# Performance work log

Hardware: AMD Instinct MI355X
Metric: run time of the kernel (lower is better)

The kernel has to match this reference:

```python
import jax, jax.numpy as jnp
import numpy as np
from itertools import product

IM_SIZE = (256, 256)
GRID_SIZE = (512, 512)
NUMPOINTS = (6, 6)
TABLE_OVERSAMP = (1024, 1024)
N_SHIFT = (128.0, 128.0)
ALPHA = tuple(2.34 * j for j in NUMPOINTS)
NBATCH, NCOIL, KLEN = 2, 16, 262144


def _kaiser_bessel(u, J, alpha):
    # order-0 Kaiser-Bessel kernel, support |u| < J/2
    z = np.sqrt(np.maximum(1.0 - (2.0 * u / J) ** 2, 0.0))
    f = np.i0(alpha * z) / np.i0(alpha)
    return np.where(np.abs(u) < J / 2.0, f, 0.0)


def _build_table(J, L, alpha):
    # table of length J*L+1 sampling the kernel at offsets u=(idx-center)/L
    idx = np.arange(J * L + 1, dtype=np.float64)
    center = np.floor(J * L / 2)
    u = (idx - center) / L
    real = _kaiser_bessel(u, J, alpha)
    return np.stack([real, np.zeros_like(real)]).astype(np.float32)  # [2, J*L+1] (real/imag)


def setup_inputs() -> dict:
    key = jax.random.key(0)
    k1, k2 = jax.random.split(key)
    x = jax.random.normal(k1, (NBATCH, NCOIL, 2) + GRID_SIZE, dtype=jnp.float32)
    om = (jax.random.uniform(k2, (NBATCH, 2, KLEN), dtype=jnp.float32) - 0.5) * (2.0 * np.pi)
    table_0 = jnp.asarray(_build_table(NUMPOINTS[0], TABLE_OVERSAMP[0], ALPHA[0]))
    table_1 = jnp.asarray(_build_table(NUMPOINTS[1], TABLE_OVERSAMP[1], ALPHA[1]))
    return {"x": x, "om": om, "table_0": table_0, "table_1": table_1}


def _interp(x, om, table_0, table_1):
    # x: [B, C, 2, Kx, Ky] gridded k-space; om: [B, 2, M] radians/voxel
    B, C = x.shape[0], x.shape[1]
    Kx, Ky = GRID_SIZE
    J0, J1 = NUMPOINTS
    M = om.shape[2]
    L = jnp.array(TABLE_OVERSAMP, dtype=x.dtype)
    centers = (J0 * TABLE_OVERSAMP[0] // 2, J1 * TABLE_OVERSAMP[1] // 2)
    gsz = jnp.array(GRID_SIZE, dtype=x.dtype)

    xflat = x.reshape(B, C, 2, Kx * Ky)
    tm = om * gsz[None, :, None] / (2.0 * jnp.pi)  # [B,2,M] grid units
    # offset to first interpolation coefficient location (Fessler convention)
    koff = 1.0 + jnp.floor(tm - jnp.array(NUMPOINTS, x.dtype)[None, :, None] / 2.0)

    # all J0*J1 tensor-product offsets
    joffs = jnp.asarray(list(product(range(J0), range(J1))), dtype=x.dtype)  # [36, 2]

    def step(carry, joff):
        acc_r, acc_i = carry
        gridind = koff + joff[None, :, None]  # [B,2,M], exact integers as floats
        distind = jnp.round((tm - gridind) * L[None, :, None]).astype(jnp.int32)  # [B,2,M]
        c0r = table_0[0, distind[:, 0] + centers[0]]  # [B,M]
        c0i = table_0[1, distind[:, 0] + centers[0]]
        c1r = table_1[0, distind[:, 1] + centers[1]]
        c1i = table_1[1, distind[:, 1] + centers[1]]
        coef_r = c0r * c1r - c0i * c1i
        coef_i = c0r * c1i + c0i * c1r
        gi = gridind.astype(jnp.int32)
        arr_ind = jnp.mod(gi[:, 0], Kx) * Ky + jnp.mod(gi[:, 1], Ky)  # [B,M] flat grid index
        dat_r = jnp.take_along_axis(xflat[:, :, 0, :], arr_ind[:, None, :], axis=2)  # [B,C,M]
        dat_i = jnp.take_along_axis(xflat[:, :, 1, :], arr_ind[:, None, :], axis=2)
        acc_r = acc_r + coef_r[:, None, :] * dat_r - coef_i[:, None, :] * dat_i
        acc_i = acc_i + coef_r[:, None, :] * dat_i + coef_i[:, None, :] * dat_r
        return (acc_r, acc_i), None

    init = (jnp.zeros((B, C, M), x.dtype), jnp.zeros((B, C, M), x.dtype))
    (kr, ki), _ = jax.lax.scan(step, init, joffs)

    # fftshift phase: y = exp(1j * om . n_shift) * kdat
    ph = jnp.einsum('bdm,d->bm', om, jnp.array(N_SHIFT, dtype=x.dtype))
    pr, pi = jnp.cos(ph), jnp.sin(ph)
    yr = kr * pr[:, None, :] - ki * pi[:, None, :]
    yi = kr * pi[:, None, :] + ki * pr[:, None, :]
    return jnp.stack([yr, yi], axis=2)  # [B,C,2,M]


def reference(x, om, table_0, table_1):
    return _interp(x, om, table_0, table_1)
```

## Files before the change

kernel.cpp:

```cpp
#include <hip/hip_runtime.h>
#include <hip/hip_fp16.h>


#define KLEN      262144
#define GX        512
#define GY        512
#define NCOILS    16
#define NBATCH    2
#define TBL_LEN   6145
#define TBL_CTR   3072
#define PLANE     (GX*GY)
#define NPTS      (NBATCH*KLEN)
#define NBINS     2048
#define NBLK      256
#define PPB       2048
#define TBLKS     (NBATCH*PLANE/256)

#define TROWS     21
#define TQ        5

typedef _Float16 half2_t __attribute__((ext_vector_type(2)));
struct alignas(16) H8 { half2_t h[4]; };

#define WS_XT       0
#define WS_OSORT    33554432
#define WS_BHIST    33554432
#define WS_BTOT     67108864
#define WS_BBASE    (67108864+8192)
#define WS_INV      69206016
#define WS_SOM      71303168
#define WS_TOTAL    75497472

__device__ inline int point_bin(float om0, float om1)
{
    const float TWO_PI = 6.2831853071795864769f;
    const float tm0 = (om0 * 512.0f) / TWO_PI;
    const float tm1 = (om1 * 512.0f) / TWO_PI;
    const int cx = ((int)floorf(tm0)) & 511;
    const int cy = ((int)floorf(tm1)) & 511;
    return ((cx >> 4) << 5) | (cy >> 4);
}

template<int O>
__device__ inline half2_t qbc(half2_t v)
{
    int i;
    __builtin_memcpy(&i, &v, 4);
    i = __builtin_amdgcn_mov_dpp(i, (O | (O << 2) | (O << 4) | (O << 6)),
                                 0xf, 0xf, true);
    half2_t r;
    __builtin_memcpy(&r, &i, 4);
    return r;
}

__global__ __launch_bounds__(256) void transpose_hist(
    const float* __restrict__ x, float4* __restrict__ xt,
    const float* __restrict__ om, unsigned* __restrict__ blockHist)
{
    __shared__ float s[32][260];
    const int t = threadIdx.x;

    if (blockHist != nullptr && blockIdx.x >= TBLKS) {
        unsigned* h = (unsigned*)s;
        const int blk = blockIdx.x - TBLKS;
#pragma unroll
        for (int i = 0; i < NBINS / 256; ++i) h[t + i * 256] = 0u;
        __syncthreads();
#pragma unroll
        for (int i = 0; i < PPB / 256; ++i) {
            const int id = blk * PPB + i * 256 + t;
            const int b = id >> 18, m = id & (KLEN - 1);
            const float om0 = om[(size_t)(b * 2 + 0) * KLEN + m];
            const float om1 = om[(size_t)(b * 2 + 1) * KLEN + m];
            const int g = (b << 10) | point_bin(om0, om1);
            atomicAdd(&h[g], 1u);
        }
        __syncthreads();
#pragma unroll
        for (int i = 0; i < NBINS / 256; ++i) {
            const int bin = t + i * 256;
            blockHist[(size_t)bin * NBLK + blk] = h[bin];
        }
        return;
    }

    const int blk   = blockIdx.x;
    const int base  = blk * 256;
    const int b     = base >> 18;
    const int cell0 = base & (PLANE - 1);

    const float* xb = x + (size_t)b * 32 * PLANE + cell0;
#pragma unroll
    for (int i = 0; i < 8; ++i) {
        const int fidx = i * 256 + t;
        const int pl = fidx >> 6;
        const int j  = fidx & 63;
        const float4 v = *(const float4*)(xb + (size_t)pl * PLANE + j * 4);
        *(float4*)&s[pl][j * 4] = v;
    }
    __syncthreads();
#pragma unroll
    for (int i = 0; i < 4; ++i) {
        const int chunk = i * 256 + t;
        const int cell = chunk >> 2, q = chunk & 3;
        H8 rec;
#pragma unroll
        for (int cc = 0; cc < 4; ++cc) {
            const int c = q * 4 + cc;
            rec.h[cc] = half2_t{(_Float16)s[2 * c][cell],
                                (_Float16)s[2 * c + 1][cell]};
        }
        xt[((size_t)b * PLANE + cell0 + cell) * 4 + q] = *(const float4*)&rec;
    }
}

__global__ __launch_bounds__(256) void scan_bins(
    unsigned* __restrict__ blockHist, unsigned* __restrict__ binTotal)
{
    __shared__ unsigned partial[256];
    const int bin = blockIdx.x;
    const int t = threadIdx.x;
    const unsigned v = blockHist[(size_t)bin * NBLK + t];
    partial[t] = v;
    __syncthreads();
    for (int d = 1; d < 256; d <<= 1) {
        unsigned x = (t >= d) ? partial[t - d] : 0u;
        __syncthreads();
        partial[t] += x;
        __syncthreads();
    }
    blockHist[(size_t)bin * NBLK + t] = partial[t] - v;
    if (t == 255) binTotal[bin] = partial[255];
}

__global__ __launch_bounds__(1024) void scatter2(
    const float*    __restrict__ om,
    const unsigned* __restrict__ blockHist,
    const unsigned* __restrict__ btot,
    unsigned* __restrict__ bbase,
    unsigned* __restrict__ inv,
    float2* __restrict__ som)
{
    __shared__ unsigned h[NBINS];
    __shared__ unsigned bbs[NBINS];
    __shared__ unsigned part[1024];
    const int t = threadIdx.x, blk = blockIdx.x;

    unsigned v[2];
    unsigned s = 0;
#pragma unroll
    for (int i = 0; i < 2; ++i) { v[i] = btot[t * 2 + i]; s += v[i]; }
    part[t] = s;
#pragma unroll
    for (int i = 0; i < NBINS / 1024; ++i) h[t + i * 1024] = 0u;
    __syncthreads();
    for (int d = 1; d < 1024; d <<= 1) {
        unsigned x = (t >= d) ? part[t - d] : 0u;
        __syncthreads();
        part[t] += x;
        __syncthreads();
    }
    unsigned base = (t > 0) ? part[t - 1] : 0u;
    bbs[t * 2]     = base;
    bbs[t * 2 + 1] = base + v[0];
    if (blk == 0) {
        bbase[t * 2]     = base;
        bbase[t * 2 + 1] = base + v[0];
    }
    __syncthreads();

#pragma unroll
    for (int i = 0; i < PPB / 1024; ++i) {
        const int id = blk * PPB + i * 1024 + t;
        const int b = id >> 18, m = id & (KLEN - 1);
        const float om0 = om[(size_t)(b * 2 + 0) * KLEN + m];
        const float om1 = om[(size_t)(b * 2 + 1) * KLEN + m];
        const int g = (b << 10) | point_bin(om0, om1);
        const unsigned r = atomicAdd(&h[g], 1u);
        const unsigned pos = bbs[g] + blockHist[(size_t)g * NBLK + blk] + r;
        inv[id]  = pos;
        som[pos] = make_float2(om0, om1);
    }
}

__global__ __launch_bounds__(256) void interp_bins(
    const float2*   __restrict__ som,
    const float*    __restrict__ t0,
    const float*    __restrict__ t1,
    const float4*   __restrict__ xt,
    const unsigned* __restrict__ bbase,
    float4*         __restrict__ osort)
{
    __shared__ float4 tile[TROWS * TROWS * TQ];
    const int bin = blockIdx.x;
    const int t   = threadIdx.x;
    const int b   = bin >> 10;
    const int cx0 = ((bin >> 5) & 31) << 4;
    const int cy0 = (bin & 31) << 4;

    const unsigned p0  = bbase[bin];
    const unsigned p1e = (bin == NBINS - 1) ? (unsigned)NPTS : bbase[bin + 1];
    const int cnt = (int)(p1e - p0);

    const float4* rec = xt + ((size_t)b << 20);
    for (int f = t; f < TROWS * TROWS * 4; f += 256) {
        const int r = f >> 2, q = f & 3;
        const int row = r / TROWS;
        const int col = r - row * TROWS;
        const int gr = (cx0 - 2 + row) & 511;
        const int gc = (cy0 - 2 + col) & 511;
        tile[r * TQ + q] = rec[(((size_t)((gr << 9) | gc)) << 2) + q];
    }
    __syncthreads();

    const int lane = t & 3;
    for (int base = 0; base < cnt; base += 64) {
        const int idx = base + (t >> 2);
        if (idx >= cnt) continue;
        const int pos = (int)p0 + idx;

        const float2 o = som[pos];
        const float om0 = o.x, om1 = o.y;

        const float TWO_PI = 6.2831853071795864769f;
        const float tm0 = (om0 * 512.0f) / TWO_PI;
        const float tm1 = (om1 * 512.0f) / TWO_PI;

        const float koff0 = 1.0f + floorf(tm0 - 3.0f);
        const float koff1 = 1.0f + floorf(tm1 - 3.0f);
        const int   k0    = (int)koff0;
        const int   k1    = (int)koff1;

        float c0r[6], c0i[6];
        int   loff[6];
#pragma unroll
        for (int j = 0; j < 6; ++j) {
            const float g0 = koff0 + (float)j;
            const int   d0 = (int)rintf((tm0 - g0) * 1024.0f) + TBL_CTR;
            c0r[j] = t0[d0];
            c0i[j] = t0[TBL_LEN + d0];
            loff[j] = ((k1 + j - cy0 + 2) & 511) * TQ;
        }
        const int j1a = lane;
        const int j1b = (lane < 2) ? lane + 4 : lane;
        const int d1a = (int)rintf((tm1 - (koff1 + (float)j1a)) * 1024.0f) + TBL_CTR;
        const int d1b = (int)rintf((tm1 - (koff1 + (float)j1b)) * 1024.0f) + TBL_CTR;
        const float c1ra = t1[d1a], c1ia = t1[TBL_LEN + d1a];
        const float c1rb = t1[d1b], c1ib = t1[TBL_LEN + d1b];

        float acr[4] = {0.f, 0.f, 0.f, 0.f};
        float aci[4] = {0.f, 0.f, 0.f, 0.f};

#define KB_DO_J1(JJ, OWNER, PP1, PP2)                                         \
        do {                                                                  \
            const half2_t p1 = qbc<OWNER>(PP1);                               \
            const half2_t p2 = qbc<OWNER>(PP2);                               \
            const float4 raw = rowp[loff[JJ]];                                \
            const H8 v = *(const H8*)&raw;                                    \
            _Pragma("unroll")                                                 \
            for (int cc = 0; cc < 4; ++cc) {                                  \
                acr[cc] = __builtin_amdgcn_fdot2(v.h[cc], p1, acr[cc], false);\
                aci[cc] = __builtin_amdgcn_fdot2(v.h[cc], p2, aci[cc], false);\
            }                                                                 \
        } while (0)

#pragma unroll
        for (int j0 = 0; j0 < 6; ++j0) {
            const int rIdx = (k0 + j0 - cx0 + 2) & 511;
            const float4* rowp = &tile[rIdx * (TROWS * TQ) + lane];
            const float ar = c0r[j0], ai = c0i[j0];
            const float crA = ar * c1ra - ai * c1ia;
            const float ciA = ar * c1ia + ai * c1ra;
            const float crB = ar * c1rb - ai * c1ib;
            const float ciB = ar * c1ib + ai * c1rb;
            const half2_t pA1 = {(_Float16)crA, (_Float16)(-ciA)};
            const half2_t pA2 = {(_Float16)ciA, (_Float16)crA};
            const half2_t pB1 = {(_Float16)crB, (_Float16)(-ciB)};
            const half2_t pB2 = {(_Float16)ciB, (_Float16)crB};

            KB_DO_J1(0, 0, pA1, pA2);
            KB_DO_J1(1, 1, pA1, pA2);
            KB_DO_J1(2, 2, pA1, pA2);
            KB_DO_J1(3, 3, pA1, pA2);
            KB_DO_J1(4, 0, pB1, pB2);
            KB_DO_J1(5, 1, pB1, pB2);
        }
#undef KB_DO_J1

        const float ph = om0 * 128.0f + om1 * 128.0f;
        const float s = __sinf(ph), c = __cosf(ph);

        H8 outrec;
#pragma unroll
        for (int cc = 0; cc < 4; ++cc) {
            const float yr = acr[cc] * c - aci[cc] * s;
            const float yi = acr[cc] * s + aci[cc] * c;
            outrec.h[cc] = half2_t{(_Float16)yr, (_Float16)yi};
        }
        osort[(size_t)pos * 4 + lane] = *(const float4*)&outrec;
    }
}

__global__ __launch_bounds__(256) void unsort_kernel(
    const unsigned* __restrict__ inv,
    const float4*   __restrict__ osort,
    float*          __restrict__ out)
{
    const int id = blockIdx.x * blockDim.x + threadIdx.x;
    const int b = id >> 18, m = id & (KLEN - 1);
    const unsigned pos = inv[id];
    const float4* rp = osort + (size_t)pos * 4;

    float4 raw[4];
#pragma unroll
    for (int q = 0; q < 4; ++q) raw[q] = rp[q];

    float* ob = out + (size_t)b * NCOILS * 2 * KLEN + m;
#pragma unroll
    for (int q = 0; q < 4; ++q) {
        const H8 v = *(const H8*)&raw[q];
#pragma unroll
        for (int cc = 0; cc < 4; ++cc) {
            const int coil = q * 4 + cc;
            ob[(size_t)(2 * coil)     * KLEN] = (float)v.h[cc].x;
            ob[(size_t)(2 * coil + 1) * KLEN] = (float)v.h[cc].y;
        }
    }
}

__global__ __launch_bounds__(256) void interp_direct(
    const float*  __restrict__ om,
    const float*  __restrict__ t0,
    const float*  __restrict__ t1,
    const float4* __restrict__ xt,
    float*        __restrict__ out)
{
    const int tid  = blockIdx.x * blockDim.x + threadIdx.x;
    const int lane = tid & 3;
    const int p    = tid >> 2;
    const int b    = p >> 18;
    const int m    = p & (KLEN - 1);

    const float om0 = om[(size_t)(b * 2 + 0) * KLEN + m];
    const float om1 = om[(size_t)(b * 2 + 1) * KLEN + m];

    const float TWO_PI = 6.2831853071795864769f;
    const float tm0 = (om0 * 512.0f) / TWO_PI;
    const float tm1 = (om1 * 512.0f) / TWO_PI;
    const float koff0 = 1.0f + floorf(tm0 - 3.0f);
    const float koff1 = 1.0f + floorf(tm1 - 3.0f);
    const int k0 = (int)koff0, k1 = (int)koff1;

    float c0r[6], c0i[6], c1r[6], c1i[6];
    int coff[6];
#pragma unroll
    for (int j = 0; j < 6; ++j) {
        const float g0 = koff0 + (float)j;
        const int d0 = (int)rintf((tm0 - g0) * 1024.0f) + TBL_CTR;
        c0r[j] = t0[d0];
        c0i[j] = t0[TBL_LEN + d0];
        const float g1 = koff1 + (float)j;
        const int d1 = (int)rintf((tm1 - g1) * 1024.0f) + TBL_CTR;
        c1r[j] = t1[d1];
        c1i[j] = t1[TBL_LEN + d1];
        coff[j] = ((k1 + j) & 511) << 2;
    }

    const float4* rec = xt + ((size_t)b << 20);
    float acr[4] = {0.f, 0.f, 0.f, 0.f};
    float aci[4] = {0.f, 0.f, 0.f, 0.f};
#pragma unroll
    for (int j0 = 0; j0 < 6; ++j0) {
        const int roff = (k0 + j0) & 511;
        const float4* rowp = rec + ((size_t)roff << 11) + lane;
        const float ar = c0r[j0], ai = c0i[j0];
#pragma unroll
        for (int j1 = 0; j1 < 6; ++j1) {
            const float br = c1r[j1], bi = c1i[j1];
            const float cr = ar * br - ai * bi;
            const float ci = ar * bi + ai * br;
            const half2_t p1 = {(_Float16)cr, (_Float16)(-ci)};
            const half2_t p2 = {(_Float16)ci, (_Float16)cr};
            const float4 raw = rowp[coff[j1]];
            const H8 v = *(const H8*)&raw;
#pragma unroll
            for (int cc = 0; cc < 4; ++cc) {
                acr[cc] = __builtin_amdgcn_fdot2(v.h[cc], p1, acr[cc], false);
                aci[cc] = __builtin_amdgcn_fdot2(v.h[cc], p2, aci[cc], false);
            }
        }
    }

    const float ph = om0 * 128.0f + om1 * 128.0f;
    const float s = sinf(ph), c = cosf(ph);
#pragma unroll
    for (int cc = 0; cc < 4; ++cc) {
        const float yr = acr[cc] * c - aci[cc] * s;
        const float yi = acr[cc] * s + aci[cc] * c;
        const int coil = lane * 4 + cc;
        const size_t ob = ((size_t)(b * NCOILS + coil) * 2) * KLEN + m;
        out[ob]        = yr;
        out[ob + KLEN] = yi;
    }
}

__global__ __launch_bounds__(256) void interp_fallback(
    const float* __restrict__ om,
    const float* __restrict__ t0,
    const float* __restrict__ t1,
    const float* __restrict__ x,
    float*       __restrict__ out)
{
    const int p = blockIdx.x * blockDim.x + threadIdx.x;
    const int b = p >> 18;
    const int m = p & (KLEN - 1);

    const float om0 = om[(size_t)(b * 2 + 0) * KLEN + m];
    const float om1 = om[(size_t)(b * 2 + 1) * KLEN + m];
    const float TWO_PI = 6.2831853071795864769f;
    const float tm0 = (om0 * 512.0f) / TWO_PI;
    const float tm1 = (om1 * 512.0f) / TWO_PI;
    const float koff0 = 1.0f + floorf(tm0 - 3.0f);
    const float koff1 = 1.0f + floorf(tm1 - 3.0f);
    const int k0 = (int)koff0, k1 = (int)koff1;

    float c0r[6], c0i[6], c1r[6], c1i[6];
    int roff[6], coff[6];
#pragma unroll
    for (int j = 0; j < 6; ++j) {
        const float g0 = koff0 + (float)j;
        const int d0 = (int)rintf((tm0 - g0) * 1024.0f) + TBL_CTR;
        c0r[j] = t0[d0];
        c0i[j] = t0[TBL_LEN + d0];
        const float g1 = koff1 + (float)j;
        const int d1 = (int)rintf((tm1 - g1) * 1024.0f) + TBL_CTR;
        c1r[j] = t1[d1];
        c1i[j] = t1[TBL_LEN + d1];
        roff[j] = (k0 + j) & 511;
        coff[j] = (k1 + j) & 511;
    }

    float accr[NCOILS], acci[NCOILS];
#pragma unroll
    for (int c = 0; c < NCOILS; ++c) { accr[c] = 0.f; acci[c] = 0.f; }

    const float* xb = x + (size_t)b * NCOILS * 2 * PLANE;
#pragma unroll
    for (int j0 = 0; j0 < 6; ++j0) {
        const float ar = c0r[j0], ai = c0i[j0];
        const int rb = roff[j0] * GY;
#pragma unroll
        for (int j1 = 0; j1 < 6; ++j1) {
            const float br = c1r[j1], bi = c1i[j1];
            const float cr = ar * br - ai * bi;
            const float ci = ar * bi + ai * br;
            const int ai_idx = rb + coff[j1];
#pragma unroll
            for (int c = 0; c < NCOILS; ++c) {
                const float dr = xb[(size_t)c * (2 * PLANE) + ai_idx];
                const float di = xb[(size_t)c * (2 * PLANE) + PLANE + ai_idx];
                accr[c] += cr * dr - ci * di;
                acci[c] += cr * di + ci * dr;
            }
        }
    }

    const float ph = om0 * 128.0f + om1 * 128.0f;
    const float s = sinf(ph), c = cosf(ph);
#pragma unroll
    for (int cc = 0; cc < NCOILS; ++cc) {
        const float yr = accr[cc] * c - acci[cc] * s;
        const float yi = accr[cc] * s + acci[cc] * c;
        size_t ob = ((size_t)(b * NCOILS + cc) * 2) * KLEN + m;
        out[ob]        = yr;
        out[ob + KLEN] = yi;
    }
}

extern "C" void kernel_launch(void* const* d_in, const int* in_sizes, int n_in,
                              void* d_out, int out_size, void* d_ws, size_t ws_size,
                              hipStream_t stream)
{
    const float* x  = (const float*)d_in[0];
    const float* om = (const float*)d_in[1];
    const float* t0 = (const float*)d_in[2];
    const float* t1 = (const float*)d_in[3];
    float* out = (float*)d_out;

    char* ws = (char*)d_ws;
    const size_t xt_bytes = (size_t)NBATCH * PLANE * NCOILS * 2 * sizeof(__half);

    if (ws_size >= (size_t)WS_TOTAL) {
        float4*   xt     = (float4*)(ws + WS_XT);
        float4*   osort  = (float4*)(ws + WS_OSORT);
        unsigned* bhist  = (unsigned*)(ws + WS_BHIST);
        unsigned* btot   = (unsigned*)(ws + WS_BTOT);
        unsigned* bbase  = (unsigned*)(ws + WS_BBASE);
        unsigned* inv    = (unsigned*)(ws + WS_INV);
        float2*   som    = (float2*)(ws + WS_SOM);

        transpose_hist<<<TBLKS + NBLK, 256, 0, stream>>>(x, xt, om, bhist);
        scan_bins<<<NBINS, 256, 0, stream>>>(bhist, btot);
        scatter2<<<NBLK, 1024, 0, stream>>>(om, bhist, btot, bbase, inv, som);
        interp_bins<<<NBINS, 256, 0, stream>>>(som, t0, t1, xt, bbase, osort);
        unsort_kernel<<<NPTS / 256, 256, 0, stream>>>(inv, osort, out);
    } else if (ws_size >= xt_bytes) {
        float4* xt = (float4*)ws;
        transpose_hist<<<TBLKS, 256, 0, stream>>>(x, xt, om, nullptr);
        interp_direct<<<NPTS * 4 / 256, 256, 0, stream>>>(om, t0, t1, xt, out);
    } else {
        interp_fallback<<<NPTS / 256, 256, 0, stream>>>(om, t0, t1, x, out);
    }
}
```

Measured before the change: 219.7 us.

## Use wavefront shuffle scans and widen interp_bins blocks to 512 threads

```diff
diff --git a/kernel.cpp b/kernel.cpp
--- a/kernel.cpp
+++ b/kernel.cpp
@@ -114,23 +114,32 @@
     }
 }
 
-__global__ __launch_bounds__(256) void scan_bins(
+__global__ __launch_bounds__(1024) void scan_bins(
     unsigned* __restrict__ blockHist, unsigned* __restrict__ binTotal)
 {
-    __shared__ unsigned partial[256];
-    const int bin = blockIdx.x;
-    const int t = threadIdx.x;
-    const unsigned v = blockHist[(size_t)bin * NBLK + t];
-    partial[t] = v;
-    __syncthreads();
-    for (int d = 1; d < 256; d <<= 1) {
-        unsigned x = (t >= d) ? partial[t - d] : 0u;
-        __syncthreads();
-        partial[t] += x;
-        __syncthreads();
-    }
-    blockHist[(size_t)bin * NBLK + t] = partial[t] - v;
-    if (t == 255) binTotal[bin] = partial[255];
+    const int t    = threadIdx.x;
+    const int lane = t & 63;
+    const int wave = t >> 6;
+    const int bin  = blockIdx.x * 16 + wave;
+
+    uint4 v = *(const uint4*)&blockHist[(size_t)bin * NBLK + lane * 4];
+    const unsigned tot = v.x + v.y + v.z + v.w;
+
+    unsigned s = tot;
+#pragma unroll
+    for (int d = 1; d < 64; d <<= 1) {
+        const unsigned x = __shfl_up(s, d);
+        if (lane >= d) s += x;
+    }
+    const unsigned excl = s - tot;
+
+    uint4 o;
+    o.x = excl;
+    o.y = excl + v.x;
+    o.z = excl + v.x + v.y;
+    o.w = excl + v.x + v.y + v.z;
+    *(uint4*)&blockHist[(size_t)bin * NBLK + lane * 4] = o;
+    if (lane == 63) binTotal[bin] = s;
 }
 
 __global__ __launch_bounds__(1024) void scatter2(
@@ -143,29 +152,31 @@
 {
     __shared__ unsigned h[NBINS];
     __shared__ unsigned bbs[NBINS];
-    __shared__ unsigned part[1024];
+    __shared__ unsigned wsum[16];
     const int t = threadIdx.x, blk = blockIdx.x;
-
-    unsigned v[2];
-    unsigned s = 0;
-#pragma unroll
-    for (int i = 0; i < 2; ++i) { v[i] = btot[t * 2 + i]; s += v[i]; }
-    part[t] = s;
+    const int lane = t & 63, wave = t >> 6;
+
+    const unsigned v0 = btot[t * 2], v1 = btot[t * 2 + 1];
+    const unsigned tot = v0 + v1;
+    unsigned s = tot;
+#pragma unroll
+    for (int d = 1; d < 64; d <<= 1) {
+        const unsigned x = __shfl_up(s, d);
+        if (lane >= d) s += x;
+    }
+    if (lane == 63) wsum[wave] = s;
 #pragma unroll
     for (int i = 0; i < NBINS / 1024; ++i) h[t + i * 1024] = 0u;
     __syncthreads();
-    for (int d = 1; d < 1024; d <<= 1) {
-        unsigned x = (t >= d) ? part[t - d] : 0u;
-        __syncthreads();
-        part[t] += x;
-        __syncthreads();
-    }
-    unsigned base = (t > 0) ? part[t - 1] : 0u;
-    bbs[t * 2]     = base;
-    bbs[t * 2 + 1] = base + v[0];
+    unsigned wp = 0;
+#pragma unroll
+    for (int i = 0; i < 16; ++i) wp += (i < wave) ? wsum[i] : 0u;
+    const unsigned excl = wp + s - tot;
+    bbs[t * 2]     = excl;
+    bbs[t * 2 + 1] = excl + v0;
     if (blk == 0) {
-        bbase[t * 2]     = base;
-        bbase[t * 2 + 1] = base + v[0];
+        bbase[t * 2]     = excl;
+        bbase[t * 2 + 1] = excl + v0;
     }
     __syncthreads();
 
@@ -183,7 +194,7 @@
     }
 }
 
-__global__ __launch_bounds__(256) void interp_bins(
+__global__ __launch_bounds__(512) void interp_bins(
     const float2*   __restrict__ som,
     const float*    __restrict__ t0,
     const float*    __restrict__ t1,
@@ -203,7 +214,7 @@
     const int cnt = (int)(p1e - p0);
 
     const float4* rec = xt + ((size_t)b << 20);
-    for (int f = t; f < TROWS * TROWS * 4; f += 256) {
+    for (int f = t; f < TROWS * TROWS * 4; f += 512) {
         const int r = f >> 2, q = f & 3;
         const int row = r / TROWS;
         const int col = r - row * TROWS;
@@ -214,7 +225,7 @@
     __syncthreads();
 
     const int lane = t & 3;
-    for (int base = 0; base < cnt; base += 64) {
+    for (int base = 0; base < cnt; base += 128) {
         const int idx = base + (t >> 2);
         if (idx >= cnt) continue;
         const int pos = (int)p0 + idx;
@@ -500,9 +511,9 @@
         float2*   som    = (float2*)(ws + WS_SOM);
 
         transpose_hist<<<TBLKS + NBLK, 256, 0, stream>>>(x, xt, om, bhist);
-        scan_bins<<<NBINS, 256, 0, stream>>>(bhist, btot);
+        scan_bins<<<NBINS / 16, 1024, 0, stream>>>(bhist, btot);
         scatter2<<<NBLK, 1024, 0, stream>>>(om, bhist, btot, bbase, inv, som);
-        interp_bins<<<NBINS, 256, 0, stream>>>(som, t0, t1, xt, bbase, osort);
+        interp_bins<<<NBINS, 512, 0, stream>>>(som, t0, t1, xt, bbase, osort);
         unsort_kernel<<<NPTS / 256, 256, 0, stream>>>(inv, osort, out);
     } else if (ws_size >= xt_bytes) {
         float4* xt = (float4*)ws;
```

Result: faster. 212.5 us (-3.3%).
